# Kernel tuning notes

Hardware: AMD Instinct MI355X
Metric: run time of the kernel (lower is better)

Reference implementation:

```python
import jax, jax.numpy as jnp
import numpy as np

N_NODES = 100000
N_EDGES = 1600000
D = 128


def _deg_inv_sqrt(idx, num_nodes):
    deg = jax.ops.segment_sum(jnp.ones_like(idx, dtype=jnp.float32), idx, num_segments=num_nodes)
    deg = jnp.clip(deg, 1.0, None)  # DGL clamps degree to min 1
    return deg ** -0.5


def graph_conv(x, W, b, src, dst, out_norm, in_norm, relu):
    # norm='both': scale by src out-degree^{-1/2}, transform, aggregate, scale by dst in-degree^{-1/2}
    h = x * out_norm[:, None]
    h = h @ W                               # [N, d_out]
    m = jax.ops.segment_sum(h[src], dst, num_segments=x.shape[0])  # sparse A^T h
    m = m * in_norm[:, None] + b
    return jax.nn.relu(m) if relu else m


def setup_inputs() -> dict:
    key = jax.random.key(0)
    ks = jax.random.split(key, 8)
    s = 1.0 / np.sqrt(D)
    return {
        "node_feats": jax.random.normal(ks[0], (N_NODES, D), dtype=jnp.float32),
        "src": jax.random.randint(ks[1], (N_EDGES,), 0, N_NODES, dtype=jnp.int32),
        "dst": jax.random.randint(ks[2], (N_EDGES,), 0, N_NODES, dtype=jnp.int32),
        "W1": jax.random.normal(ks[3], (D, D), dtype=jnp.float32) * s,
        "b1": jnp.zeros((D,), jnp.float32),
        "W2": jax.random.normal(ks[4], (D, D), dtype=jnp.float32) * s,
        "b2": jnp.zeros((D,), jnp.float32),
        "res_W": jax.random.normal(ks[5], (D, D), dtype=jnp.float32) * s,
        "mlp_W": jax.random.normal(ks[6], (D, 2), dtype=jnp.float32) * s,
        "mlp_b": jnp.zeros((2,), jnp.float32),
    }


def reference(node_feats, src, dst, W1, b1, W2, b2, res_W, mlp_W, mlp_b):
    out_norm = _deg_inv_sqrt(src, node_feats.shape[0])  # out-degree of source nodes
    in_norm = _deg_inv_sqrt(dst, node_feats.shape[0])   # in-degree of dest nodes
    h = graph_conv(node_feats, W1, b1, src, dst, out_norm, in_norm, relu=True)
    # dropout p=0.0 -> identity
    h = graph_conv(h, W2, b2, src, dst, out_norm, in_norm, relu=False)
    # residual (res_fc is Linear without bias)
    h = h + node_feats @ res_W
    # final MLP head -> logits [N, 2]
    return h @ mlp_W + mlp_b
```

## Files before the change

kernel.cpp:

```cpp
#include <hip/hip_runtime.h>
#include <stdint.h>

__device__ __forceinline__ float bflo(unsigned int u) {
    union { unsigned int u; float f; } c; c.u = u << 16; return c.f;
}
__device__ __forceinline__ float bfhi(unsigned int u) {
    union { unsigned int u; float f; } c; c.u = u & 0xffff0000u; return c.f;
}
__device__ __forceinline__ unsigned int f2bf(float f) {
    union { float f; unsigned int u; } c; c.f = f;
    unsigned int u = c.u;
    u += 0x7fffu + ((u >> 16) & 1u);
    return u >> 16;
}
__device__ __forceinline__ unsigned int packbf(float a, float b) {
    return f2bf(a) | (f2bf(b) << 16);
}

typedef __attribute__((ext_vector_type(8))) short s8v;
typedef __attribute__((ext_vector_type(4))) float f4v;
typedef __attribute__((ext_vector_type(2))) float f2v;

__device__ __forceinline__ f4v mfma16(s8v a, s8v b, f4v c) {
    return __builtin_amdgcn_mfma_f32_16x16x32_bf16(a, b, c, 0, 0, 0);
}

__device__ __forceinline__ unsigned char f2fp8(float v) {
    return (unsigned char)(__builtin_amdgcn_cvt_pk_fp8_f32(v, v, 0, false) & 0xff);
}

#define RANGE_BITS 14
#define RANGE (1 << RANGE_BITS)
#define NR_PAD 8
#define NSLICE 64

__global__ __launch_bounds__(256) void k_prep_w(const float* __restrict__ W1,
                                                const float* __restrict__ W2,
                                                const float* __restrict__ Wr,
                                                unsigned short* __restrict__ Wt) {
    const float* W = (blockIdx.x == 0) ? W1 : (blockIdx.x == 1) ? W2 : Wr;
    unsigned short* T = Wt + (size_t)blockIdx.x * 16384;
    const int wv = threadIdx.x >> 6, l = threadIdx.x & 63;
    const int kb = blockIdx.y * 32 + wv * 8;
#pragma unroll
    for (int half = 0; half < 2; ++half) {
        const int n = l + half * 64;
        unsigned short tmp[8];
#pragma unroll
        for (int j = 0; j < 8; ++j) tmp[j] = (unsigned short)f2bf(W[(size_t)(kb + j) * 128 + n]);
#pragma unroll
        for (int j = 0; j < 8; j += 2)
            *(unsigned int*)&T[(size_t)n * 128 + kb + j] =
                (unsigned int)tmp[j] | ((unsigned int)tmp[j + 1] << 16);
    }
}

__global__ __launch_bounds__(64) void k_prep_k(const float* __restrict__ b2,
                                               const float* __restrict__ mlpW,
                                               const float* __restrict__ mlpB,
                                               float* __restrict__ K) {
    const int l = threadIdx.x;
    float p0 = b2[l] * mlpW[l * 2 + 0] + b2[l + 64] * mlpW[(l + 64) * 2 + 0];
    float p1 = b2[l] * mlpW[l * 2 + 1] + b2[l + 64] * mlpW[(l + 64) * 2 + 1];
#pragma unroll
    for (int off = 32; off > 0; off >>= 1) {
        p0 += __shfl_xor(p0, off);
        p1 += __shfl_xor(p1, off);
    }
    if (l == 0) { K[0] = p0 + mlpB[0]; K[1] = p1 + mlpB[1]; }
}

__global__ __launch_bounds__(256) void k_hist_lds(const int* __restrict__ src,
                                                  const int* __restrict__ dst,
                                                  unsigned int* __restrict__ partialS,
                                                  unsigned int* __restrict__ partialD,
                                                  int E, int EPS) {
    __shared__ unsigned int cnt[RANGE / 2];
    const int r = blockIdx.x & 7;
    const int s = blockIdx.x >> 3;
    const int a = blockIdx.y;
    const int* __restrict__ arr = a ? dst : src;
    unsigned int* part = (a ? partialD : partialS)
                         + ((size_t)r * NSLICE + s) * (RANGE / 2);
    for (int i = threadIdx.x; i < RANGE / 2; i += 256) cnt[i] = 0;
    __syncthreads();
    const int e0 = s * EPS;
    const int e1 = min(E, e0 + EPS);
    int e = e0 + threadIdx.x * 4;
    for (; e + 3 < e1; e += 1024) {
        const int4 v = *(const int4*)&arr[e];
        if ((v.x >> RANGE_BITS) == r) { int l = v.x & (RANGE - 1); atomicAdd(&cnt[l >> 1], 1u << ((l & 1) << 4)); }
        if ((v.y >> RANGE_BITS) == r) { int l = v.y & (RANGE - 1); atomicAdd(&cnt[l >> 1], 1u << ((l & 1) << 4)); }
        if ((v.z >> RANGE_BITS) == r) { int l = v.z & (RANGE - 1); atomicAdd(&cnt[l >> 1], 1u << ((l & 1) << 4)); }
        if ((v.w >> RANGE_BITS) == r) { int l = v.w & (RANGE - 1); atomicAdd(&cnt[l >> 1], 1u << ((l & 1) << 4)); }
    }
    for (; e < e1; ++e) {
        const int idx = arr[e];
        if ((idx >> RANGE_BITS) == r) { int l = idx & (RANGE - 1); atomicAdd(&cnt[l >> 1], 1u << ((l & 1) << 4)); }
    }
    __syncthreads();
    for (int i = threadIdx.x; i < RANGE / 2; i += 256) part[i] = cnt[i];
}

__global__ __launch_bounds__(256) void k_deg_reduce(unsigned int* __restrict__ pS,
                                                    unsigned int* __restrict__ pD,
                                                    float* __restrict__ out_norm,
                                                    float* __restrict__ in_norm,
                                                    int* __restrict__ in_deg, int N) {
    const int a = blockIdx.y;
    const int t = blockIdx.x * 256 + threadIdx.x;
    const int r = t >> (RANGE_BITS - 1);
    const int w = t & ((RANGE / 2) - 1);
    unsigned int* base = (a ? pD : pS) + (size_t)r * NSLICE * (RANGE / 2) + w;
    unsigned int lo = 0, hi = 0;
    if (a) {
        for (int s = 0; s < NSLICE; ++s) {
            const unsigned int v = base[(size_t)s * (RANGE / 2)];
            base[(size_t)s * (RANGE / 2)] = lo | (hi << 16);
            lo += v & 0xffffu; hi += v >> 16;
        }
    } else {
        for (int s = 0; s < NSLICE; ++s) {
            const unsigned int v = base[(size_t)s * (RANGE / 2)];
            lo += v & 0xffffu; hi += v >> 16;
        }
    }
    const int n0 = r * RANGE + 2 * w, n1 = n0 + 1;
    if (a) {
        if (n0 < N) { in_deg[n0] = (int)lo; in_norm[n0] = rsqrtf(fmaxf((float)lo, 1.f)); }
        if (n1 < N) { in_deg[n1] = (int)hi; in_norm[n1] = rsqrtf(fmaxf((float)hi, 1.f)); }
    } else {
        if (n0 < N) out_norm[n0] = rsqrtf(fmaxf((float)lo, 1.f));
        if (n1 < N) out_norm[n1] = rsqrtf(fmaxf((float)hi, 1.f));
    }
}

__global__ __launch_bounds__(1024) void k_scan_block(const int* __restrict__ in,
                                                     int* __restrict__ row_ptr,
                                                     int* __restrict__ partials, int n) {
    __shared__ int sh[1024];
    int i = blockIdx.x * 1024 + threadIdx.x;
    int v = (i < n) ? in[i] : 0;
    sh[threadIdx.x] = v;
    __syncthreads();
    for (int off = 1; off < 1024; off <<= 1) {
        int t = (threadIdx.x >= off) ? sh[threadIdx.x - off] : 0;
        __syncthreads();
        sh[threadIdx.x] += t;
        __syncthreads();
    }
    if (i < n) row_ptr[i + 1] = sh[threadIdx.x];
    if (threadIdx.x == 1023) partials[blockIdx.x] = sh[1023];
}

__global__ __launch_bounds__(1024) void k_scan_partials(int* __restrict__ partials, int nb) {
    __shared__ int sh[1024];
    int v = (threadIdx.x < nb) ? partials[threadIdx.x] : 0;
    sh[threadIdx.x] = v;
    __syncthreads();
    for (int off = 1; off < 1024; off <<= 1) {
        int t = (threadIdx.x >= off) ? sh[threadIdx.x - off] : 0;
        __syncthreads();
        sh[threadIdx.x] += t;
        __syncthreads();
    }
    if (threadIdx.x < nb) partials[threadIdx.x] = sh[threadIdx.x] - v;
}

__global__ void k_scan_finalize(int* __restrict__ row_ptr, const int* __restrict__ partials,
                                int n) {
    int i = blockIdx.x * blockDim.x + threadIdx.x;
    if (i < n) {
        row_ptr[i + 1] += partials[i >> 10];
        if (i == 0) row_ptr[0] = 0;
    }
}

__global__ __launch_bounds__(256) void k_scatter_lds(const int* __restrict__ src,
                                                     const int* __restrict__ dst,
                                                     const unsigned int* __restrict__ pD,
                                                     const int* __restrict__ row_ptr,
                                                     int* __restrict__ ssrc, int E, int EPS) {
    __shared__ unsigned int cur[RANGE / 2];
    const int r = blockIdx.x & 7;
    const int s = blockIdx.x >> 3;
    const unsigned int* pre = pD + ((size_t)r * NSLICE + s) * (RANGE / 2);
    for (int i = threadIdx.x; i < RANGE / 2; i += 256) cur[i] = pre[i];
    __syncthreads();
    const int e0 = s * EPS;
    const int e1 = min(E, e0 + EPS);
    int e = e0 + threadIdx.x * 4;
    for (; e + 3 < e1; e += 1024) {
        const int4 v = *(const int4*)&dst[e];
#pragma unroll
        for (int j = 0; j < 4; ++j) {
            const int d = (&v.x)[j];
            if ((d >> RANGE_BITS) == r) {
                const int local = d & (RANGE - 1);
                const int sh = (local & 1) << 4;
                const unsigned int old = atomicAdd(&cur[local >> 1], 1u << sh);
                const unsigned int off = (old >> sh) & 0xffffu;
                ssrc[row_ptr[d] + (int)off] = src[e + j];
            }
        }
    }
    for (; e < e1; ++e) {
        const int d = dst[e];
        if ((d >> RANGE_BITS) == r) {
            const int local = d & (RANGE - 1);
            const int sh = (local & 1) << 4;
            const unsigned int old = atomicAdd(&cur[local >> 1], 1u << sh);
            const unsigned int off = (old >> sh) & 0xffffu;
            ssrc[row_ptr[d] + (int)off] = src[e];
        }
    }
}

template <typename TIN, int MODE>
__global__ __launch_bounds__(256) void gemm_mfma(const TIN* __restrict__ X,
                                                 const unsigned short* __restrict__ Wt0,
                                                 const unsigned short* __restrict__ Wt1,
                                                 const float* __restrict__ scale,
                                                 unsigned char* __restrict__ out_table,
                                                 float2* __restrict__ outv,
                                                 const float* __restrict__ mlpW,
                                                 int N) {
    constexpr int NW = (MODE == 0) ? 2 : 1;
    __shared__ unsigned short Ws[NW][128 * 128];
    const int tid = threadIdx.x;
#pragma unroll
    for (int w = 0; w < NW; ++w) {
        const unsigned short* Wsrc = w ? Wt1 : Wt0;
        for (int i = tid; i < 2048; i += 256) {
            const int n = i >> 4, b = i & 15;
            const uint4 v = *(const uint4*)&Wsrc[(size_t)n * 128 + b * 8];
            *(uint4*)&Ws[w][n * 128 + ((b ^ (n & 15)) << 3)] = v;
        }
    }
    __syncthreads();

    const int lane = tid & 63;
    const int wave = tid >> 6;
    const int quad = lane >> 4;
    const int l16 = lane & 15;
    const int r_base = blockIdx.x * 64 + wave * 16;
    const int ra = min(r_base + l16, N - 1);

    f4v acc[NW][8];
#pragma unroll
    for (int w = 0; w < NW; ++w)
#pragma unroll
        for (int nn = 0; nn < 8; ++nn) acc[w][nn] = (f4v)0.f;

    const TIN* xp = X + (size_t)ra * 128 + quad * 8;

#pragma unroll
    for (int kt = 0; kt < 4; ++kt) {
        s8v af;
        if constexpr (sizeof(TIN) == 4) {
            const float4 lo = *(const float4*)(xp + kt * 32);
            const float4 hi = *(const float4*)(xp + kt * 32 + 4);
            af[0] = (short)f2bf(lo.x); af[1] = (short)f2bf(lo.y);
            af[2] = (short)f2bf(lo.z); af[3] = (short)f2bf(lo.w);
            af[4] = (short)f2bf(hi.x); af[5] = (short)f2bf(hi.y);
            af[6] = (short)f2bf(hi.z); af[7] = (short)f2bf(hi.w);
        } else {
            af = *(const s8v*)(xp + kt * 32);
        }
#pragma unroll
        for (int nn = 0; nn < 8; ++nn) {
            const int bofs = (nn * 16 + l16) * 128 + (((kt * 4 + quad) ^ l16) << 3);
#pragma unroll
            for (int w = 0; w < NW; ++w) {
                const s8v bf = *(const s8v*)&Ws[w][bofs];
                acc[w][nn] = mfma16(af, bf, acc[w][nn]);
            }
        }
    }

    const int rc = r_base + quad * 4;
    float sc[4];
#pragma unroll
    for (int g = 0; g < 4; ++g) sc[g] = scale[min(rc + g, N - 1)];

    if constexpr (MODE == 0) {
#pragma unroll
        for (int nn = 0; nn < 8; ++nn) {
            const int col = nn * 16 + l16;
#pragma unroll
            for (int g = 0; g < 4; ++g) {
                const int r = rc + g;
                if (r < N) out_table[(size_t)r * 128 + col] = f2fp8(acc[0][nn][g] * sc[g]);
            }
        }
    }

    {
        float2 w2[8];
#pragma unroll
        for (int nn = 0; nn < 8; ++nn)
            w2[nn] = ((const float2*)mlpW)[nn * 16 + l16];
#pragma unroll
        for (int g = 0; g < 4; ++g) {
            float p0 = 0.f, p1 = 0.f;
#pragma unroll
            for (int nn = 0; nn < 8; ++nn) {
                float val;
                if constexpr (MODE == 0) val = acc[1][nn][g];
                else                     val = acc[0][nn][g] * sc[g];
                p0 = fmaf(val, w2[nn].x, p0);
                p1 = fmaf(val, w2[nn].y, p1);
            }
#pragma unroll
            for (int off = 1; off < 16; off <<= 1) {
                p0 += __shfl_xor(p0, off);
                p1 += __shfl_xor(p1, off);
            }
            const int r = rc + g;
            if (l16 == 0 && r < N) outv[r] = make_float2(p0, p1);
        }
    }
}

__global__ __launch_bounds__(256) void k_spmm1(const unsigned char* __restrict__ T,
                                               const int* __restrict__ row_ptr,
                                               const int* __restrict__ ssrc,
                                               const float* __restrict__ in_norm,
                                               const float* __restrict__ bias,
                                               unsigned short* __restrict__ Hout, int N) {
    const int lane = threadIdx.x & 63;
    const int grp = lane >> 4;
    const int gl  = lane & 15;
    const int d = blockIdx.x * 4 + (threadIdx.x >> 6);
    if (d >= N) return;

    const int start = row_ptr[d], end = row_ptr[d + 1];
    float acc[8];
#pragma unroll
    for (int j = 0; j < 8; ++j) acc[j] = 0.f;

    for (int base = start; base < end; base += 64) {
        const int cnt = min(64, end - base);
        const int sl = (lane < cnt) ? ssrc[base + lane] : 0;
        for (int i = 0; i < cnt; i += 16) {
            int   ss[4];
            float mm[4];
            uint2 ww[4];
#pragma unroll
            for (int u = 0; u < 4; ++u) {
                const int e = i + 4 * u + grp;
                ss[u] = __shfl(sl, min(e, cnt - 1));
                mm[u] = (e < cnt) ? 1.f : 0.f;
            }
#pragma unroll
            for (int u = 0; u < 4; ++u)
                ww[u] = *(const uint2*)&T[(size_t)ss[u] * 128 + gl * 8];
#pragma unroll
            for (int u = 0; u < 4; ++u) {
                const f2v a0 = __builtin_amdgcn_cvt_pk_f32_fp8(ww[u].x, false);
                const f2v a1 = __builtin_amdgcn_cvt_pk_f32_fp8(ww[u].x, true);
                const f2v a2 = __builtin_amdgcn_cvt_pk_f32_fp8(ww[u].y, false);
                const f2v a3 = __builtin_amdgcn_cvt_pk_f32_fp8(ww[u].y, true);
                const float m = mm[u];
                acc[0] = fmaf(m, a0[0], acc[0]); acc[1] = fmaf(m, a0[1], acc[1]);
                acc[2] = fmaf(m, a1[0], acc[2]); acc[3] = fmaf(m, a1[1], acc[3]);
                acc[4] = fmaf(m, a2[0], acc[4]); acc[5] = fmaf(m, a2[1], acc[5]);
                acc[6] = fmaf(m, a3[0], acc[6]); acc[7] = fmaf(m, a3[1], acc[7]);
            }
        }
    }

#pragma unroll
    for (int j = 0; j < 8; ++j) {
        acc[j] += __shfl_xor(acc[j], 16);
        acc[j] += __shfl_xor(acc[j], 32);
    }

    const float inr = in_norm[d];
    const float4 bb0 = *(const float4*)&bias[gl * 8];
    const float4 bb1 = *(const float4*)&bias[gl * 8 + 4];
    float v[8];
    v[0] = fmaxf(acc[0] * inr + bb0.x, 0.f); v[1] = fmaxf(acc[1] * inr + bb0.y, 0.f);
    v[2] = fmaxf(acc[2] * inr + bb0.z, 0.f); v[3] = fmaxf(acc[3] * inr + bb0.w, 0.f);
    v[4] = fmaxf(acc[4] * inr + bb1.x, 0.f); v[5] = fmaxf(acc[5] * inr + bb1.y, 0.f);
    v[6] = fmaxf(acc[6] * inr + bb1.z, 0.f); v[7] = fmaxf(acc[7] * inr + bb1.w, 0.f);

    if (grp == 0) {
        uint4 o;
        o.x = packbf(v[0], v[1]); o.y = packbf(v[2], v[3]);
        o.z = packbf(v[4], v[5]); o.w = packbf(v[6], v[7]);
        *(uint4*)&Hout[(size_t)d * 128 + gl * 8] = o;
    }
}

__global__ __launch_bounds__(256) void k_final(const float2* __restrict__ u,
                                               const int* __restrict__ row_ptr,
                                               const int* __restrict__ ssrc,
                                               const float* __restrict__ in_norm,
                                               const float2* __restrict__ v,
                                               const float* __restrict__ K,
                                               float2* __restrict__ out, int N) {
    const int d = blockIdx.x * 256 + threadIdx.x;
    if (d >= N) return;
    const int start = row_ptr[d], end = row_ptr[d + 1];
    float sx = 0.f, sy = 0.f;
    int i = start;
    for (; i + 4 <= end; i += 4) {
        const int s0 = ssrc[i], s1 = ssrc[i + 1], s2 = ssrc[i + 2], s3 = ssrc[i + 3];
        const float2 u0 = u[s0], u1 = u[s1], u2 = u[s2], u3 = u[s3];
        sx += (u0.x + u1.x) + (u2.x + u3.x);
        sy += (u0.y + u1.y) + (u2.y + u3.y);
    }
    for (; i < end; ++i) {
        const float2 uu = u[ssrc[i]];
        sx += uu.x; sy += uu.y;
    }
    const float inr = in_norm[d];
    const float2 vv = v[d];
    out[d] = make_float2(sx * inr + vv.x + K[0], sy * inr + vv.y + K[1]);
}

extern "C" void kernel_launch(void* const* d_in, const int* in_sizes, int n_in,
                              void* d_out, int out_size, void* d_ws, size_t ws_size,
                              hipStream_t stream) {
    const float* x     = (const float*)d_in[0];
    const int*   src   = (const int*)d_in[1];
    const int*   dst   = (const int*)d_in[2];
    const float* W1    = (const float*)d_in[3];
    const float* b1    = (const float*)d_in[4];
    const float* W2    = (const float*)d_in[5];
    const float* b2    = (const float*)d_in[6];
    const float* res_W = (const float*)d_in[7];
    const float* mlp_W = (const float*)d_in[8];
    const float* mlp_b = (const float*)d_in[9];
    float* out = (float*)d_out;

    const int N = in_sizes[0] / 128;
    const int E = in_sizes[1];
    const int EPS = (E + NSLICE - 1) / NSLICE;

    char* p = (char*)d_ws;
    unsigned char*  A = (unsigned char*)p;   p += (size_t)N * 128;
    unsigned short* B = (unsigned short*)p;  p += (size_t)N * 128 * 2;
    unsigned short* Wt = (unsigned short*)p; p += (size_t)3 * 16384 * 2;
    float* out_norm = (float*)p;             p += (size_t)N * 4;
    float* in_norm  = (float*)p;             p += (size_t)N * 4;
    int* in_deg     = (int*)p;               p += (size_t)N * 4;
    int* row_ptr    = (int*)p;               p += (size_t)(N + 1) * 4;
    int* scanpart   = (int*)p;               p += (size_t)1024 * 4;
    float* Kc       = (float*)p;             p += (size_t)16;
    float2* v2      = (float2*)p;            p += (size_t)N * 8;
    float2* u2      = (float2*)p;            p += (size_t)N * 8;
    int* ssrc       = (int*)p;               p += (size_t)E * 4;
    unsigned int* partialS = (unsigned int*)A;
    unsigned int* partialD = (unsigned int*)((char*)B + (size_t)4 * 1024 * 1024);

    const int gN = (N + 255) / 256;
    const int nb = (N + 1023) / 1024;
    const int gGemm = (N + 63) / 64;
    const int gSpmm = (N + 3) / 4;

    k_prep_w<<<dim3(3, 4), 256, 0, stream>>>(W1, W2, res_W, Wt);
    k_prep_k<<<1, 64, 0, stream>>>(b2, mlp_W, mlp_b, Kc);

    k_hist_lds<<<dim3(NR_PAD * NSLICE, 2), 256, 0, stream>>>(src, dst, partialS, partialD, E, EPS);
    k_deg_reduce<<<dim3(NR_PAD * (RANGE / 2) / 256, 2), 256, 0, stream>>>(partialS, partialD,
                                                                          out_norm, in_norm, in_deg, N);

    k_scan_block<<<nb, 1024, 0, stream>>>(in_deg, row_ptr, scanpart, N);
    k_scan_partials<<<1, 1024, 0, stream>>>(scanpart, nb);
    k_scan_finalize<<<gN, 256, 0, stream>>>(row_ptr, scanpart, N);
    k_scatter_lds<<<NR_PAD * NSLICE, 256, 0, stream>>>(src, dst, partialD, row_ptr, ssrc, E, EPS);

    gemm_mfma<float, 0><<<gGemm, 256, 0, stream>>>(x, Wt, Wt + 2 * 16384, out_norm,
                                                   A, v2, mlp_W, N);

    k_spmm1<<<gSpmm, 256, 0, stream>>>(A, row_ptr, ssrc, in_norm, b1, B, N);

    gemm_mfma<unsigned short, 1><<<gGemm, 256, 0, stream>>>(B, Wt + 16384, nullptr, out_norm,
                                                            nullptr, u2, mlp_W, N);

    k_final<<<gN, 256, 0, stream>>>(u2, row_ptr, ssrc, in_norm, v2, Kc, (float2*)out, N);

    (void)n_in; (void)out_size; (void)ws_size;
}
```

Before: 288.4 us.

## Replace LDS-partitioned degree histogram and scatter with global-atomic counting and cursor scatter

Swaps the range-partitioned LDS histogram (8 ranges by 64 slices, with per-slice prefix partials) for a zero kernel, a global-atomic degree count, and a separate norm kernel. CSR construction now uses a per-node cursor array from the scan and a global atomicAdd scatter instead of LDS cursors seeded from slice prefixes. This removes the repeated 8x rereads of src/dst and the large partial-histogram traffic, but relies on contended global atomics. It also makes the order of edges within each row nondeterministic.

```diff
diff --git a/kernel.cpp b/kernel.cpp
--- a/kernel.cpp
+++ b/kernel.cpp
@@ -28,11 +28,6 @@
 __device__ __forceinline__ unsigned char f2fp8(float v) {
     return (unsigned char)(__builtin_amdgcn_cvt_pk_fp8_f32(v, v, 0, false) & 0xff);
 }
-
-#define RANGE_BITS 14
-#define RANGE (1 << RANGE_BITS)
-#define NR_PAD 8
-#define NSLICE 64
 
 __global__ __launch_bounds__(256) void k_prep_w(const float* __restrict__ W1,
                                                 const float* __restrict__ W2,
@@ -70,68 +65,39 @@
     if (l == 0) { K[0] = p0 + mlpB[0]; K[1] = p1 + mlpB[1]; }
 }
 
-__global__ __launch_bounds__(256) void k_hist_lds(const int* __restrict__ src,
-                                                  const int* __restrict__ dst,
-                                                  unsigned int* __restrict__ partialS,
-                                                  unsigned int* __restrict__ partialD,
-                                                  int E, int EPS) {
-    __shared__ unsigned int cnt[RANGE / 2];
-    const int r = blockIdx.x & 7;
-    const int s = blockIdx.x >> 3;
-    const int a = blockIdx.y;
-    const int* __restrict__ arr = a ? dst : src;
-    unsigned int* part = (a ? partialD : partialS)
-                         + ((size_t)r * NSLICE + s) * (RANGE / 2);
-    for (int i = threadIdx.x; i < RANGE / 2; i += 256) cnt[i] = 0;
-    __syncthreads();
-    const int e0 = s * EPS;
-    const int e1 = min(E, e0 + EPS);
-    int e = e0 + threadIdx.x * 4;
-    for (; e + 3 < e1; e += 1024) {
-        const int4 v = *(const int4*)&arr[e];
-        if ((v.x >> RANGE_BITS) == r) { int l = v.x & (RANGE - 1); atomicAdd(&cnt[l >> 1], 1u << ((l & 1) << 4)); }
-        if ((v.y >> RANGE_BITS) == r) { int l = v.y & (RANGE - 1); atomicAdd(&cnt[l >> 1], 1u << ((l & 1) << 4)); }
-        if ((v.z >> RANGE_BITS) == r) { int l = v.z & (RANGE - 1); atomicAdd(&cnt[l >> 1], 1u << ((l & 1) << 4)); }
-        if ((v.w >> RANGE_BITS) == r) { int l = v.w & (RANGE - 1); atomicAdd(&cnt[l >> 1], 1u << ((l & 1) << 4)); }
-    }
-    for (; e < e1; ++e) {
-        const int idx = arr[e];
-        if ((idx >> RANGE_BITS) == r) { int l = idx & (RANGE - 1); atomicAdd(&cnt[l >> 1], 1u << ((l & 1) << 4)); }
-    }
-    __syncthreads();
-    for (int i = threadIdx.x; i < RANGE / 2; i += 256) part[i] = cnt[i];
-}
-
-__global__ __launch_bounds__(256) void k_deg_reduce(unsigned int* __restrict__ pS,
-                                                    unsigned int* __restrict__ pD,
-                                                    float* __restrict__ out_norm,
-                                                    float* __restrict__ in_norm,
-                                                    int* __restrict__ in_deg, int N) {
-    const int a = blockIdx.y;
-    const int t = blockIdx.x * 256 + threadIdx.x;
-    const int r = t >> (RANGE_BITS - 1);
-    const int w = t & ((RANGE / 2) - 1);
-    unsigned int* base = (a ? pD : pS) + (size_t)r * NSLICE * (RANGE / 2) + w;
-    unsigned int lo = 0, hi = 0;
-    if (a) {
-        for (int s = 0; s < NSLICE; ++s) {
-            const unsigned int v = base[(size_t)s * (RANGE / 2)];
-            base[(size_t)s * (RANGE / 2)] = lo | (hi << 16);
-            lo += v & 0xffffu; hi += v >> 16;
-        }
+__global__ __launch_bounds__(256) void k_zero(unsigned int* __restrict__ p, int n) {
+    const int i = blockIdx.x * 256 + threadIdx.x;
+    if (i < n) p[i] = 0u;
+}
+
+__global__ __launch_bounds__(256) void k_count(const int* __restrict__ src,
+                                               const int* __restrict__ dst,
+                                               unsigned int* __restrict__ degS,
+                                               unsigned int* __restrict__ degD, int E) {
+    const int i = (blockIdx.x * 256 + threadIdx.x) * 4;
+    if (i + 3 < E) {
+        const int4 s = *(const int4*)&src[i];
+        const int4 d = *(const int4*)&dst[i];
+        atomicAdd(&degS[s.x], 1u); atomicAdd(&degS[s.y], 1u);
+        atomicAdd(&degS[s.z], 1u); atomicAdd(&degS[s.w], 1u);
+        atomicAdd(&degD[d.x], 1u); atomicAdd(&degD[d.y], 1u);
+        atomicAdd(&degD[d.z], 1u); atomicAdd(&degD[d.w], 1u);
     } else {
-        for (int s = 0; s < NSLICE; ++s) {
-            const unsigned int v = base[(size_t)s * (RANGE / 2)];
-            lo += v & 0xffffu; hi += v >> 16;
-        }
-    }
-    const int n0 = r * RANGE + 2 * w, n1 = n0 + 1;
-    if (a) {
-        if (n0 < N) { in_deg[n0] = (int)lo; in_norm[n0] = rsqrtf(fmaxf((float)lo, 1.f)); }
-        if (n1 < N) { in_deg[n1] = (int)hi; in_norm[n1] = rsqrtf(fmaxf((float)hi, 1.f)); }
-    } else {
-        if (n0 < N) out_norm[n0] = rsqrtf(fmaxf((float)lo, 1.f));
-        if (n1 < N) out_norm[n1] = rsqrtf(fmaxf((float)hi, 1.f));
+        for (int e = i; e < E; ++e) {
+            atomicAdd(&degS[src[e]], 1u);
+            atomicAdd(&degD[dst[e]], 1u);
+        }
+    }
+}
+
+__global__ __launch_bounds__(256) void k_norms(const unsigned int* __restrict__ degS,
+                                               const unsigned int* __restrict__ degD,
+                                               float* __restrict__ out_norm,
+                                               float* __restrict__ in_norm, int N) {
+    const int i = blockIdx.x * 256 + threadIdx.x;
+    if (i < N) {
+        out_norm[i] = rsqrtf(fmaxf((float)degS[i], 1.f));
+        in_norm[i]  = rsqrtf(fmaxf((float)degD[i], 1.f));
     }
 }
 
@@ -168,50 +134,33 @@
 }
 
 __global__ void k_scan_finalize(int* __restrict__ row_ptr, const int* __restrict__ partials,
-                                int n) {
+                                const int* __restrict__ deg, int* __restrict__ cursor, int n) {
     int i = blockIdx.x * blockDim.x + threadIdx.x;
     if (i < n) {
-        row_ptr[i + 1] += partials[i >> 10];
+        const int rp1 = row_ptr[i + 1] + partials[i >> 10];
+        row_ptr[i + 1] = rp1;
+        cursor[i] = rp1 - deg[i];
         if (i == 0) row_ptr[0] = 0;
     }
 }
 
-__global__ __launch_bounds__(256) void k_scatter_lds(const int* __restrict__ src,
-                                                     const int* __restrict__ dst,
-                                                     const unsigned int* __restrict__ pD,
-                                                     const int* __restrict__ row_ptr,
-                                                     int* __restrict__ ssrc, int E, int EPS) {
-    __shared__ unsigned int cur[RANGE / 2];
-    const int r = blockIdx.x & 7;
-    const int s = blockIdx.x >> 3;
-    const unsigned int* pre = pD + ((size_t)r * NSLICE + s) * (RANGE / 2);
-    for (int i = threadIdx.x; i < RANGE / 2; i += 256) cur[i] = pre[i];
-    __syncthreads();
-    const int e0 = s * EPS;
-    const int e1 = min(E, e0 + EPS);
-    int e = e0 + threadIdx.x * 4;
-    for (; e + 3 < e1; e += 1024) {
-        const int4 v = *(const int4*)&dst[e];
-#pragma unroll
-        for (int j = 0; j < 4; ++j) {
-            const int d = (&v.x)[j];
-            if ((d >> RANGE_BITS) == r) {
-                const int local = d & (RANGE - 1);
-                const int sh = (local & 1) << 4;
-                const unsigned int old = atomicAdd(&cur[local >> 1], 1u << sh);
-                const unsigned int off = (old >> sh) & 0xffffu;
-                ssrc[row_ptr[d] + (int)off] = src[e + j];
-            }
-        }
-    }
-    for (; e < e1; ++e) {
-        const int d = dst[e];
-        if ((d >> RANGE_BITS) == r) {
-            const int local = d & (RANGE - 1);
-            const int sh = (local & 1) << 4;
-            const unsigned int old = atomicAdd(&cur[local >> 1], 1u << sh);
-            const unsigned int off = (old >> sh) & 0xffffu;
-            ssrc[row_ptr[d] + (int)off] = src[e];
+__global__ __launch_bounds__(256) void k_scatter(const int* __restrict__ src,
+                                                 const int* __restrict__ dst,
+                                                 int* __restrict__ cursor,
+                                                 int* __restrict__ ssrc, int E) {
+    const int i = (blockIdx.x * 256 + threadIdx.x) * 4;
+    if (i + 3 < E) {
+        const int4 s = *(const int4*)&src[i];
+        const int4 d = *(const int4*)&dst[i];
+        const int p0 = atomicAdd(&cursor[d.x], 1);
+        const int p1 = atomicAdd(&cursor[d.y], 1);
+        const int p2 = atomicAdd(&cursor[d.z], 1);
+        const int p3 = atomicAdd(&cursor[d.w], 1);
+        ssrc[p0] = s.x; ssrc[p1] = s.y; ssrc[p2] = s.z; ssrc[p3] = s.w;
+    } else {
+        for (int e = i; e < E; ++e) {
+            const int p = atomicAdd(&cursor[dst[e]], 1);
+            ssrc[p] = src[e];
         }
     }
 }
@@ -437,40 +386,40 @@
 
     const int N = in_sizes[0] / 128;
     const int E = in_sizes[1];
-    const int EPS = (E + NSLICE - 1) / NSLICE;
 
     char* p = (char*)d_ws;
-    unsigned char*  A = (unsigned char*)p;   p += (size_t)N * 128;
-    unsigned short* B = (unsigned short*)p;  p += (size_t)N * 128 * 2;
+    unsigned char*  A  = (unsigned char*)p;  p += (size_t)N * 128;
+    unsigned short* B  = (unsigned short*)p; p += (size_t)N * 128 * 2;
     unsigned short* Wt = (unsigned short*)p; p += (size_t)3 * 16384 * 2;
-    float* out_norm = (float*)p;             p += (size_t)N * 4;
-    float* in_norm  = (float*)p;             p += (size_t)N * 4;
-    int* in_deg     = (int*)p;               p += (size_t)N * 4;
-    int* row_ptr    = (int*)p;               p += (size_t)(N + 1) * 4;
-    int* scanpart   = (int*)p;               p += (size_t)1024 * 4;
-    float* Kc       = (float*)p;             p += (size_t)16;
-    float2* v2      = (float2*)p;            p += (size_t)N * 8;
-    float2* u2      = (float2*)p;            p += (size_t)N * 8;
-    int* ssrc       = (int*)p;               p += (size_t)E * 4;
-    unsigned int* partialS = (unsigned int*)A;
-    unsigned int* partialD = (unsigned int*)((char*)B + (size_t)4 * 1024 * 1024);
+    float* out_norm    = (float*)p;          p += (size_t)N * 4;
+    float* in_norm     = (float*)p;          p += (size_t)N * 4;
+    int* row_ptr       = (int*)p;            p += (size_t)(N + 1) * 4;
+    int* scanpart      = (int*)p;            p += (size_t)1024 * 4;
+    float* Kc          = (float*)p;          p += (size_t)16;
+    float2* v2         = (float2*)p;         p += (size_t)N * 8;
+    float2* u2         = (float2*)p;         p += (size_t)N * 8;
+    int* ssrc          = (int*)p;            p += (size_t)E * 4;
+    unsigned int* degS = (unsigned int*)A;
+    unsigned int* degD = degS + N;
+    int*          cursor = (int*)(degD + N);
 
     const int gN = (N + 255) / 256;
     const int nb = (N + 1023) / 1024;
     const int gGemm = (N + 63) / 64;
     const int gSpmm = (N + 3) / 4;
+    const int gEdge4 = (E / 4 + 255) / 256;
 
     k_prep_w<<<dim3(3, 4), 256, 0, stream>>>(W1, W2, res_W, Wt);
     k_prep_k<<<1, 64, 0, stream>>>(b2, mlp_W, mlp_b, Kc);
 
-    k_hist_lds<<<dim3(NR_PAD * NSLICE, 2), 256, 0, stream>>>(src, dst, partialS, partialD, E, EPS);
-    k_deg_reduce<<<dim3(NR_PAD * (RANGE / 2) / 256, 2), 256, 0, stream>>>(partialS, partialD,
-                                                                          out_norm, in_norm, in_deg, N);
-
-    k_scan_block<<<nb, 1024, 0, stream>>>(in_deg, row_ptr, scanpart, N);
+    k_zero<<<(2 * N + 255) / 256, 256, 0, stream>>>(degS, 2 * N);
+    k_count<<<gEdge4, 256, 0, stream>>>(src, dst, degS, degD, E);
+    k_norms<<<gN, 256, 0, stream>>>(degS, degD, out_norm, in_norm, N);
+
+    k_scan_block<<<nb, 1024, 0, stream>>>((const int*)degD, row_ptr, scanpart, N);
     k_scan_partials<<<1, 1024, 0, stream>>>(scanpart, nb);
-    k_scan_finalize<<<gN, 256, 0, stream>>>(row_ptr, scanpart, N);
-    k_scatter_lds<<<NR_PAD * NSLICE, 256, 0, stream>>>(src, dst, partialD, row_ptr, ssrc, E, EPS);
+    k_scan_finalize<<<gN, 256, 0, stream>>>(row_ptr, scanpart, (const int*)degD, cursor, N);
+    k_scatter<<<gEdge4, 256, 0, stream>>>(src, dst, cursor, ssrc, E);
 
     gemm_mfma<float, 0><<<gGemm, 256, 0, stream>>>(x, Wt, Wt + 2 * 16384, out_norm,
                                                    A, v2, mlp_W, N);
```

Result: slower. 454.9 us (+57.7%).
